# Kernel tuning notes

Measured on AMD Instinct MI355X. Metric: run time of the kernel, lower is better.

## Reference

```python
import jax, jax.numpy as jnp
import numpy as np

B, H0, W0, C = 16, 56, 56, 96
NH, WS, SS = 3, 7, 3
HID, NCL, TAU = 384, 128, 0.5
EPS = 1e-6

def layernorm(x, g, b):
    m = jnp.mean(x, -1, keepdims=True)
    v = jnp.mean((x - m) ** 2, -1, keepdims=True)
    return (x - m) * jax.lax.rsqrt(v + 1e-5) * g + b

def setup_inputs() -> dict:
    key = jax.random.key(0)
    ks = jax.random.split(key, 16)
    s = lambda d: 1.0 / np.sqrt(d)
    return {
        "x": jax.random.normal(ks[0], (B, H0 * W0, C), jnp.float32),
        "norm1_g": jnp.ones((C,)), "norm1_b": jnp.zeros((C,)),
        "qkv_w": jax.random.normal(ks[1], (3 * C, C)) * s(C),
        "qkv_b": jnp.zeros((3 * C,)),
        "proj_w": jax.random.normal(ks[2], (C, C)) * s(C),
        "proj_b": jnp.zeros((C,)),
        "norm2_g": jnp.ones((C,)), "norm2_b": jnp.zeros((C,)),
        "ffn_norm_g": jnp.ones((C,)), "ffn_norm_b": jnp.zeros((C,)),
        "pin_w": jax.random.normal(ks[3], (HID, C)) * s(C),
        "pin_b": jnp.zeros((HID,)),
        "tm_inc": jax.random.normal(ks[4], (NCL, 2 * HID)) * 0.5,
        "tm_out": jax.random.normal(ks[5], (NCL, C)) * s(NCL),
        "gate": jnp.float32(0.5),
        "H": H0, "W": W0,
    }

def window_attention(win, qkv_w, qkv_b, proj_w, proj_b):
    N, T, Cc = win.shape
    hd = Cc // NH
    qkv = win @ qkv_w.T + qkv_b                      # [N, T, 3C]
    qkv = qkv.reshape(N, T, 3, NH, hd).transpose(2, 0, 3, 1, 4)
    q, k, v = qkv[0], qkv[1], qkv[2]                 # [N, nh, T, hd]
    attn = jax.nn.softmax(jnp.einsum('nhqd,nhkd->nhqk', q, k) * (hd ** -0.5), axis=-1)
    out = jnp.einsum('nhqk,nhkd->nhqd', attn, v).transpose(0, 2, 1, 3).reshape(N, T, Cc)
    return out @ proj_w.T + proj_b

def tm_ffn(x, ffn_norm_g, ffn_norm_b, pin_w, pin_b, tm_inc, tm_out, gate):
    # x: [B, T, C]
    Bb, T, Cc = x.shape
    y = jax.nn.sigmoid(layernorm(x, ffn_norm_g, ffn_norm_b) @ pin_w.T + pin_b)  # [B,T,HID]
    flat = y.reshape(Bb * T, HID)
    lits = jnp.clip(jnp.concatenate([flat, 1.0 - flat], axis=-1), EPS, 1.0)     # [N, 2*HID]
    m = jax.nn.sigmoid(tm_inc)
    hard = (m > TAU).astype(m.dtype)
    m_ste = m + jax.lax.stop_gradient(hard - m)      # binary via STE
    # binary mask -> conjunction prod_k l_k^{m_jk} = exp(log(l) @ m^T)
    clauses = jnp.exp(jnp.log(lits) @ m_ste.T)       # [N, NCL]
    logits = (clauses @ tm_out).reshape(Bb, T, Cc)
    g = jax.nn.sigmoid(gate)
    return g * logits + (1.0 - g) * jax.nn.sigmoid(logits)

def reference(x, norm1_g, norm1_b, qkv_w, qkv_b, proj_w, proj_b,
              norm2_g, norm2_b, ffn_norm_g, ffn_norm_b,
              pin_w, pin_b, tm_inc, tm_out, gate, H, W):
    Bb, L, Cc = x.shape
    shortcut = x
    y = layernorm(x, norm1_g, norm1_b).reshape(Bb, H, W, Cc)
    pad_h = (WS - H % WS) % WS
    pad_w = (WS - W % WS) % WS
    if pad_h or pad_w:
        y = jnp.pad(y, ((0, 0), (0, pad_h), (0, pad_w), (0, 0)))
    Hp, Wp = y.shape[1], y.shape[2]
    if SS > 0:
        y = jnp.roll(y, shift=(-SS, -SS), axis=(1, 2))
    # window partition
    y = y.reshape(Bb, Hp // WS, WS, Wp // WS, WS, Cc).transpose(0, 1, 3, 2, 4, 5)
    win = y.reshape(-1, WS * WS, Cc)
    a = window_attention(win, qkv_w, qkv_b, proj_w, proj_b)
    a = a.reshape(Bb, Hp // WS, Wp // WS, WS, WS, Cc)
    if SS > 0:
        a = jnp.roll(a, shift=(SS, SS), axis=(3, 4))
    # window reverse
    a = a.transpose(0, 1, 3, 2, 4, 5).reshape(Bb, Hp, Wp, Cc)
    if pad_h or pad_w:
        a = a[:, :H, :W, :]
    a = a.reshape(Bb, H * W, Cc)
    x1 = shortcut + a
    x2 = x1 + tm_ffn(layernorm(x1, norm2_g, norm2_b),
                     ffn_norm_g, ffn_norm_b, pin_w, pin_b, tm_inc, tm_out, gate)
    return x2
```

## Files before the change

kernel.cpp:

```cpp
#include <hip/hip_runtime.h>

#define NB 16
#define NHH 56
#define NWW 56
#define NC 96
#define NL (NHH*NWW)
#define NTOK (NB*NL)
#define WSZ 7
#define NT 49
#define SSH 3
#define NWIN 1024
#define HDIM 32
#define HID_ 384
#define NCL_ 128
#define NLIT 768
#define EPS_ 1e-6f
#define LOG_EPS -13.815510558f

typedef unsigned short u16;
typedef unsigned int   u32;
typedef __attribute__((ext_vector_type(8))) short short8;
typedef __attribute__((ext_vector_type(4))) float f32x4;

__device__ __forceinline__ float us2f(u16 u) {
  union { u32 u; float f; } x; x.u = ((u32)u) << 16; return x.f;
}
__device__ __forceinline__ u16 f2us(float f) {
  union { float f; u32 u; } x; x.f = f;
  u32 lsb = (x.u >> 16) & 1u;
  return (u16)((x.u + 0x7fffu + lsb) >> 16);
}
__device__ __forceinline__ float sigmoidf_(float x) { return 1.f / (1.f + __expf(-x)); }

__global__ __launch_bounds__(256) void k0_prep(const float* __restrict__ tm_inc,
                                               const float* __restrict__ pin_w,
                                               const float* __restrict__ tm_out,
                                               const float* __restrict__ qkv_w,
                                               const float* __restrict__ proj_w,
                                               u16* __restrict__ maskb,
                                               u16* __restrict__ pinwb,
                                               u16* __restrict__ tmoT,
                                               u16* __restrict__ qkvwb,
                                               u16* __restrict__ projwb) {
  int idx = blockIdx.x * 256 + threadIdx.x;
  if (idx < NCL_ * NLIT) {
    int c = idx / NLIT, q = idx - c * NLIT;
    int j = (q & 1) ? (q >> 1) + HID_ : (q >> 1);
    maskb[idx] = (tm_inc[(size_t)c * NLIT + j] > 0.f) ? (u16)0x3F80 : (u16)0;
  }
  if (idx < HID_ * NC)
    pinwb[idx] = f2us(pin_w[idx]);
  if (idx < NC * NCL_) {
    int c = idx / NCL_, k = idx - c * NCL_;
    tmoT[idx] = f2us(tm_out[(size_t)k * NC + c]);
  }
  if (idx < 3 * NC * NC)
    qkvwb[idx] = f2us(qkv_w[idx]);
  if (idx < NC * NC)
    projwb[idx] = f2us(proj_w[idx]);
}

__global__ __launch_bounds__(256, 4) void k2_attn(const float* __restrict__ x,
                                               const float* __restrict__ n1g,
                                               const float* __restrict__ n1b,
                                               const u16* __restrict__ qkvwb,
                                               const float* __restrict__ qkv_b,
                                               const u16* __restrict__ projwb,
                                               const float* __restrict__ proj_b,
                                               float* __restrict__ x1) {
  __shared__ __align__(16) u16 syb[64 * 104];
  __shared__ __align__(16) u16 sk [64 * 104];
  __shared__ __align__(16) u16 svT[96 * 72];
  const int tid  = threadIdx.x;
  const int wave = tid >> 6;
  const int lane = tid & 63;
  const int l16  = lane & 15;
  const int quad = lane >> 4;
  const int win  = blockIdx.x;
  const int t0   = wave * 16;
  const int bb = win >> 6, wl = win & 63;
  const int hbase = (wl >> 3) * WSZ, wbase = (wl & 7) * WSZ;

  {
    const int t = tid >> 2, s = tid & 3;
    if (t < NT) {
      int hp = hbase + t / WSZ, wp = wbase + t % WSZ;
      int h = hp + SSH; if (h >= NHH) h -= NHH;
      int w = wp + SSH; if (w >= NWW) w -= NWW;
      const float* xp = x + ((size_t)bb * NL + (size_t)h * NWW + w) * NC;
      float4 v[6];
      float sum = 0.f;
      #pragma unroll
      for (int k = 0; k < 6; ++k) {
        v[k] = *reinterpret_cast<const float4*>(xp + s * 4 + k * 16);
        sum += v[k].x + v[k].y + v[k].z + v[k].w;
      }
      sum += __shfl_xor(sum, 1); sum += __shfl_xor(sum, 2);
      float mean = sum * (1.f / 96.f);
      float ssq = 0.f;
      #pragma unroll
      for (int k = 0; k < 6; ++k) {
        float d0 = v[k].x - mean, d1 = v[k].y - mean;
        float d2 = v[k].z - mean, d3 = v[k].w - mean;
        ssq += d0 * d0 + d1 * d1 + d2 * d2 + d3 * d3;
      }
      ssq += __shfl_xor(ssq, 1); ssq += __shfl_xor(ssq, 2);
      float rstd = rsqrtf(ssq * (1.f / 96.f) + 1e-5f);
      #pragma unroll
      for (int k = 0; k < 6; ++k) {
        int c = s * 4 + k * 16;
        const float4 g4 = *reinterpret_cast<const float4*>(n1g + c);
        const float4 b4 = *reinterpret_cast<const float4*>(n1b + c);
        syb[t * 104 + c + 0] = f2us((v[k].x - mean) * rstd * g4.x + b4.x);
        syb[t * 104 + c + 1] = f2us((v[k].y - mean) * rstd * g4.y + b4.y);
        syb[t * 104 + c + 2] = f2us((v[k].z - mean) * rstd * g4.z + b4.z);
        syb[t * 104 + c + 3] = f2us((v[k].w - mean) * rstd * g4.w + b4.w);
      }
    } else {
      #pragma unroll
      for (int k = 0; k < 6; ++k) {
        int c = s * 4 + k * 16;
        syb[t * 104 + c + 0] = 0; syb[t * 104 + c + 1] = 0;
        syb[t * 104 + c + 2] = 0; syb[t * 104 + c + 3] = 0;
      }
    }
  }

  {
    short8 afr[3];
    #pragma unroll
    for (int ks = 0; ks < 3; ++ks)
      afr[ks] = *reinterpret_cast<const short8*>(&syb[(t0 + l16) * 104 + quad * 8 + ks * 32]);
    short8 rb[4][3];
    #pragma unroll
    for (int p = 0; p < 4; ++p)
      #pragma unroll
      for (int ks = 0; ks < 3; ++ks)
        rb[p][ks] = *reinterpret_cast<const short8*>(
            qkvwb + (size_t)(p * 16 + l16) * NC + quad * 8 + ks * 32);
    #pragma unroll
    for (int nt = 0; nt < 18; ++nt) {
      const int n0 = nt * 16;
      const float bias = qkv_b[n0 + l16];
      short8 b0 = rb[nt & 3][0], b1 = rb[nt & 3][1], b2 = rb[nt & 3][2];
      if (nt + 4 < 18) {
        #pragma unroll
        for (int ks = 0; ks < 3; ++ks)
          rb[nt & 3][ks] = *reinterpret_cast<const short8*>(
              qkvwb + (size_t)((nt + 4) * 16 + l16) * NC + quad * 8 + ks * 32);
      }
      f32x4 acc = {0.f, 0.f, 0.f, 0.f};
      acc = __builtin_amdgcn_mfma_f32_16x16x32_bf16(afr[0], b0, acc, 0, 0, 0);
      acc = __builtin_amdgcn_mfma_f32_16x16x32_bf16(afr[1], b1, acc, 0, 0, 0);
      acc = __builtin_amdgcn_mfma_f32_16x16x32_bf16(afr[2], b2, acc, 0, 0, 0);
      const int part = nt / 6;
      const int oc = n0 - part * 96 + l16;
      if (part < 2) {
        u16* dst = (part == 0) ? syb : sk;
        #pragma unroll
        for (int r = 0; r < 4; ++r)
          dst[(t0 + quad * 4 + r) * 104 + oc] = f2us(acc[r] + bias);
      } else {
        #pragma unroll
        for (int r = 0; r < 4; ++r)
          svT[oc * 72 + (t0 + quad * 4 + r)] = f2us(acc[r] + bias);
      }
    }
  }
  __syncthreads();

  u16* spw = sk + wave * 16 * 72;
  const float sscale = 0.17677669529663687f;
  short8 qf[3];
  f32x4 s[3][4];
  #pragma unroll
  for (int h = 0; h < 3; ++h)
    qf[h] = *reinterpret_cast<const short8*>(&syb[(t0 + l16) * 104 + h * HDIM + quad * 8]);
  #pragma unroll
  for (int h = 0; h < 3; ++h) {
    const int d0 = h * HDIM;
    #pragma unroll
    for (int nt = 0; nt < 4; ++nt) {
      short8 kf = *reinterpret_cast<const short8*>(&sk[(nt * 16 + l16) * 104 + d0 + quad * 8]);
      f32x4 a = {0.f, 0.f, 0.f, 0.f};
      s[h][nt] = __builtin_amdgcn_mfma_f32_16x16x32_bf16(qf[h], kf, a, 0, 0, 0);
    }
  }
  __syncthreads();
  #pragma unroll
  for (int h = 0; h < 3; ++h) {
    const int d0 = h * HDIM;
    #pragma unroll
    for (int nt = 0; nt < 4; ++nt)
      #pragma unroll
      for (int r = 0; r < 4; ++r) s[h][nt][r] *= sscale;
    if (l16 >= 1) {
      #pragma unroll
      for (int r = 0; r < 4; ++r) s[h][3][r] = -1e30f;
    }
    #pragma unroll
    for (int r = 0; r < 4; ++r) {
      float m = fmaxf(fmaxf(s[h][0][r], s[h][1][r]), fmaxf(s[h][2][r], s[h][3][r]));
      #pragma unroll
      for (int off = 8; off > 0; off >>= 1) m = fmaxf(m, __shfl_xor(m, off, 16));
      float e0 = __expf(s[h][0][r] - m), e1 = __expf(s[h][1][r] - m);
      float e2 = __expf(s[h][2][r] - m), e3 = __expf(s[h][3][r] - m);
      float sum = e0 + e1 + e2 + e3;
      #pragma unroll
      for (int off = 8; off > 0; off >>= 1) sum += __shfl_xor(sum, off, 16);
      float inv = 1.f / sum;
      const int row = quad * 4 + r;
      spw[row * 72 +      l16] = f2us(e0 * inv);
      spw[row * 72 + 16 + l16] = f2us(e1 * inv);
      spw[row * 72 + 32 + l16] = f2us(e2 * inv);
      spw[row * 72 + 48 + l16] = f2us(e3 * inv);
    }
    short8 pa[2];
    pa[0] = *reinterpret_cast<const short8*>(&spw[l16 * 72 + quad * 8]);
    pa[1] = *reinterpret_cast<const short8*>(&spw[l16 * 72 + 32 + quad * 8]);
    #pragma unroll
    for (int nt = 0; nt < 2; ++nt) {
      const int c0 = d0 + nt * 16;
      f32x4 acc = {0.f, 0.f, 0.f, 0.f};
      #pragma unroll
      for (int ks = 0; ks < 2; ++ks) {
        short8 vb = *reinterpret_cast<const short8*>(&svT[(c0 + l16) * 72 + ks * 32 + quad * 8]);
        acc = __builtin_amdgcn_mfma_f32_16x16x32_bf16(pa[ks], vb, acc, 0, 0, 0);
      }
      #pragma unroll
      for (int r = 0; r < 4; ++r)
        syb[(t0 + quad * 4 + r) * 104 + c0 + l16] = f2us(acc[r]);
    }
  }

  {
    short8 aa[3];
    #pragma unroll
    for (int ks = 0; ks < 3; ++ks)
      aa[ks] = *reinterpret_cast<const short8*>(&syb[(t0 + l16) * 104 + quad * 8 + ks * 32]);

    size_t tokr[4]; bool tval[4];
    #pragma unroll
    for (int r = 0; r < 4; ++r) {
      const int t = t0 + quad * 4 + r;
      tval[r] = (t < NT);
      int rr = t / WSZ + SSH; if (rr >= WSZ) rr -= WSZ;
      int qq = t % WSZ + SSH; if (qq >= WSZ) qq -= WSZ;
      tokr[r] = (size_t)bb * NL + (size_t)(hbase + rr) * NWW + (wbase + qq);
    }
    float xv[6][4];
    #pragma unroll
    for (int nt = 0; nt < 6; ++nt)
      #pragma unroll
      for (int r = 0; r < 4; ++r)
        xv[nt][r] = tval[r] ? x[tokr[r] * NC + nt * 16 + l16] : 0.f;

    short8 pbr[2][3];
    #pragma unroll
    for (int ks = 0; ks < 3; ++ks)
      pbr[0][ks] = *reinterpret_cast<const short8*>(
          projwb + (size_t)l16 * NC + quad * 8 + ks * 32);
    #pragma unroll
    for (int nt = 0; nt < 6; ++nt) {
      const int n0 = nt * 16;
      const float pb = proj_b[n0 + l16];
      short8 b0 = pbr[nt & 1][0], b1 = pbr[nt & 1][1], b2 = pbr[nt & 1][2];
      if (nt + 1 < 6) {
        #pragma unroll
        for (int ks = 0; ks < 3; ++ks)
          pbr[(nt + 1) & 1][ks] = *reinterpret_cast<const short8*>(
              projwb + (size_t)((nt + 1) * 16 + l16) * NC + quad * 8 + ks * 32);
      }
      f32x4 acc = {0.f, 0.f, 0.f, 0.f};
      acc = __builtin_amdgcn_mfma_f32_16x16x32_bf16(aa[0], b0, acc, 0, 0, 0);
      acc = __builtin_amdgcn_mfma_f32_16x16x32_bf16(aa[1], b1, acc, 0, 0, 0);
      acc = __builtin_amdgcn_mfma_f32_16x16x32_bf16(aa[2], b2, acc, 0, 0, 0);
      #pragma unroll
      for (int r = 0; r < 4; ++r) {
        if (tval[r])
          x1[tokr[r] * NC + n0 + l16] = xv[nt][r] + acc[r] + pb;
      }
    }
  }
}

__device__ __forceinline__ short8 lit_pack(f32x4 p, f32x4 pbv) {
  union { short8 s; u32 w[4]; } u;
  #pragma unroll
  for (int r = 0; r < 4; ++r) {
    const float a  = p[r] + pbv[r];
    const float sp = fmaxf(a, 0.f) + __logf(1.f + __expf(-fabsf(a)));
    const u16 lo = f2us(fmaxf(a - sp, LOG_EPS));
    const u16 hi = f2us(fmaxf(-sp,    LOG_EPS));
    u.w[r] = (u32)lo | ((u32)hi << 16);
  }
  return u.s;
}

__device__ __forceinline__ void k4_step(int ks, bool pref,
    const u16* __restrict__ pinwb, const float* __restrict__ pin_b,
    const u16* __restrict__ maskb, int l16, int quad,
    short8 (&pa)[3], f32x4& pbv, short8 (&mb)[8],
    const short8 (&zb)[2][3], f32x4 (&cacc)[2][8]) {
  const short8 a0 = pa[0], a1 = pa[1], a2 = pa[2];
  const f32x4 pb = pbv;
  f32x4 p0 = {0.f, 0.f, 0.f, 0.f}, p1 = {0.f, 0.f, 0.f, 0.f};
  p0 = __builtin_amdgcn_mfma_f32_16x16x32_bf16(a0, zb[0][0], p0, 0, 0, 0);
  p1 = __builtin_amdgcn_mfma_f32_16x16x32_bf16(a0, zb[1][0], p1, 0, 0, 0);
  p0 = __builtin_amdgcn_mfma_f32_16x16x32_bf16(a1, zb[0][1], p0, 0, 0, 0);
  p1 = __builtin_amdgcn_mfma_f32_16x16x32_bf16(a1, zb[1][1], p1, 0, 0, 0);
  p0 = __builtin_amdgcn_mfma_f32_16x16x32_bf16(a2, zb[0][2], p0, 0, 0, 0);
  p1 = __builtin_amdgcn_mfma_f32_16x16x32_bf16(a2, zb[1][2], p1, 0, 0, 0);
  if (pref) {
    const u16* pp = pinwb + (size_t)((ks + 2) * 16 + l16) * NC + quad * 8;
    pa[0] = *reinterpret_cast<const short8*>(pp);
    pa[1] = *reinterpret_cast<const short8*>(pp + 32);
    pa[2] = *reinterpret_cast<const short8*>(pp + 64);
    pbv   = *reinterpret_cast<const f32x4*>(pin_b + (ks + 2) * 16 + quad * 4);
  }
  const short8 lf0 = lit_pack(p0, pb);
  const short8 lf1 = lit_pack(p1, pb);
  #pragma unroll
  for (int ct = 0; ct < 8; ++ct) {
    cacc[0][ct] = __builtin_amdgcn_mfma_f32_16x16x32_bf16(lf0, mb[ct], cacc[0][ct], 0, 0, 0);
    cacc[1][ct] = __builtin_amdgcn_mfma_f32_16x16x32_bf16(lf1, mb[ct], cacc[1][ct], 0, 0, 0);
  }
  if (pref) {
    #pragma unroll
    for (int ct = 0; ct < 8; ++ct)
      mb[ct] = *reinterpret_cast<const short8*>(
          maskb + (size_t)(ct * 16 + l16) * NLIT + (ks + 2) * 32 + quad * 8);
  }
}

__device__ __forceinline__ float sum4_(float4 v) { return (v.x + v.y) + (v.z + v.w); }

__global__ __launch_bounds__(256, 2) void k4_ffn(const float* __restrict__ x1,
                                              const float* __restrict__ g2,
                                              const float* __restrict__ b2,
                                              const float* __restrict__ gf,
                                              const float* __restrict__ bf,
                                              const u16* __restrict__ pinwb,
                                              const float* __restrict__ pin_b,
                                              const u16* __restrict__ maskb,
                                              const u16* __restrict__ tmoT,
                                              const float* __restrict__ gate,
                                              float* __restrict__ out) {
  __shared__ __align__(16) u16 claT_s[4 * 32 * 136];
  const int tid  = threadIdx.x;
  const int wave = tid >> 6;
  const int lane = tid & 63;
  const int l16  = lane & 15;
  const int quad = lane >> 4;
  u16* claT = claT_s + wave * 32 * 136;
  const size_t tok0 = (size_t)blockIdx.x * 128 + wave * 32;

  float4 g2v[3][2], b2v[3][2], gfv[3][2], bfv[3][2];
  #pragma unroll
  for (int k = 0; k < 3; ++k) {
    const int c = k * 32 + quad * 8;
    g2v[k][0] = *reinterpret_cast<const float4*>(g2 + c);
    g2v[k][1] = *reinterpret_cast<const float4*>(g2 + c + 4);
    b2v[k][0] = *reinterpret_cast<const float4*>(b2 + c);
    b2v[k][1] = *reinterpret_cast<const float4*>(b2 + c + 4);
    gfv[k][0] = *reinterpret_cast<const float4*>(gf + c);
    gfv[k][1] = *reinterpret_cast<const float4*>(gf + c + 4);
    bfv[k][0] = *reinterpret_cast<const float4*>(bf + c);
    bfv[k][1] = *reinterpret_cast<const float4*>(bf + c + 4);
  }
  short8 zb[2][3];
  #pragma unroll
  for (int g = 0; g < 2; ++g) {
    const float* xp = x1 + (tok0 + g * 16 + l16) * NC + quad * 8;
    float4 va[3], vb[3];
    float sum = 0.f;
    #pragma unroll
    for (int k = 0; k < 3; ++k) {
      va[k] = *reinterpret_cast<const float4*>(xp + k * 32);
      vb[k] = *reinterpret_cast<const float4*>(xp + k * 32 + 4);
      sum += sum4_(va[k]) + sum4_(vb[k]);
    }
    sum += __shfl_xor(sum, 16); sum += __shfl_xor(sum, 32);
    const float mean = sum * (1.f / 96.f);
    float ssq = 0.f;
    #pragma unroll
    for (int k = 0; k < 3; ++k) {
      float d;
      d = va[k].x - mean; ssq += d * d;  d = va[k].y - mean; ssq += d * d;
      d = va[k].z - mean; ssq += d * d;  d = va[k].w - mean; ssq += d * d;
      d = vb[k].x - mean; ssq += d * d;  d = vb[k].y - mean; ssq += d * d;
      d = vb[k].z - mean; ssq += d * d;  d = vb[k].w - mean; ssq += d * d;
    }
    ssq += __shfl_xor(ssq, 16); ssq += __shfl_xor(ssq, 32);
    const float rstd = rsqrtf(ssq * (1.f / 96.f) + 1e-5f);
    float sum2 = 0.f;
    #pragma unroll
    for (int k = 0; k < 3; ++k) {
      va[k].x = (va[k].x - mean) * rstd * g2v[k][0].x + b2v[k][0].x; sum2 += va[k].x;
      va[k].y = (va[k].y - mean) * rstd * g2v[k][0].y + b2v[k][0].y; sum2 += va[k].y;
      va[k].z = (va[k].z - mean) * rstd * g2v[k][0].z + b2v[k][0].z; sum2 += va[k].z;
      va[k].w = (va[k].w - mean) * rstd * g2v[k][0].w + b2v[k][0].w; sum2 += va[k].w;
      vb[k].x = (vb[k].x - mean) * rstd * g2v[k][1].x + b2v[k][1].x; sum2 += vb[k].x;
      vb[k].y = (vb[k].y - mean) * rstd * g2v[k][1].y + b2v[k][1].y; sum2 += vb[k].y;
      vb[k].z = (vb[k].z - mean) * rstd * g2v[k][1].z + b2v[k][1].z; sum2 += vb[k].z;
      vb[k].w = (vb[k].w - mean) * rstd * g2v[k][1].w + b2v[k][1].w; sum2 += vb[k].w;
    }
    sum2 += __shfl_xor(sum2, 16); sum2 += __shfl_xor(sum2, 32);
    const float mean2 = sum2 * (1.f / 96.f);
    float ssq2 = 0.f;
    #pragma unroll
    for (int k = 0; k < 3; ++k) {
      float d;
      d = va[k].x - mean2; ssq2 += d * d;  d = va[k].y - mean2; ssq2 += d * d;
      d = va[k].z - mean2; ssq2 += d * d;  d = va[k].w - mean2; ssq2 += d * d;
      d = vb[k].x - mean2; ssq2 += d * d;  d = vb[k].y - mean2; ssq2 += d * d;
      d = vb[k].z - mean2; ssq2 += d * d;  d = vb[k].w - mean2; ssq2 += d * d;
    }
    ssq2 += __shfl_xor(ssq2, 16); ssq2 += __shfl_xor(ssq2, 32);
    const float rstd2 = rsqrtf(ssq2 * (1.f / 96.f) + 1e-5f);
    #pragma unroll
    for (int k = 0; k < 3; ++k) {
      const float z0 = (va[k].x - mean2) * rstd2 * gfv[k][0].x + bfv[k][0].x;
      const float z1 = (va[k].y - mean2) * rstd2 * gfv[k][0].y + bfv[k][0].y;
      const float z2 = (va[k].z - mean2) * rstd2 * gfv[k][0].z + bfv[k][0].z;
      const float z3 = (va[k].w - mean2) * rstd2 * gfv[k][0].w + bfv[k][0].w;
      const float z4 = (vb[k].x - mean2) * rstd2 * gfv[k][1].x + bfv[k][1].x;
      const float z5 = (vb[k].y - mean2) * rstd2 * gfv[k][1].y + bfv[k][1].y;
      const float z6 = (vb[k].z - mean2) * rstd2 * gfv[k][1].z + bfv[k][1].z;
      const float z7 = (vb[k].w - mean2) * rstd2 * gfv[k][1].w + bfv[k][1].w;
      union { short8 s; u32 w[4]; } uz;
      uz.w[0] = (u32)f2us(z0) | ((u32)f2us(z1) << 16);
      uz.w[1] = (u32)f2us(z2) | ((u32)f2us(z3) << 16);
      uz.w[2] = (u32)f2us(z4) | ((u32)f2us(z5) << 16);
      uz.w[3] = (u32)f2us(z6) | ((u32)f2us(z7) << 16);
      zb[g][k] = uz.s;
    }
  }

  short8 paA[3], paB[3], mbA[8], mbB[8];
  f32x4 pbvA, pbvB;
  {
    const u16* pp0 = pinwb + (size_t)(l16) * NC + quad * 8;
    const u16* pp1 = pinwb + (size_t)(16 + l16) * NC + quad * 8;
    #pragma unroll
    for (int k = 0; k < 3; ++k) {
      paA[k] = *reinterpret_cast<const short8*>(pp0 + k * 32);
      paB[k] = *reinterpret_cast<const short8*>(pp1 + k * 32);
    }
    pbvA = *reinterpret_cast<const f32x4*>(pin_b + quad * 4);
    pbvB = *reinterpret_cast<const f32x4*>(pin_b + 16 + quad * 4);
    #pragma unroll
    for (int ct = 0; ct < 8; ++ct) {
      const u16* mp = maskb + (size_t)(ct * 16 + l16) * NLIT + quad * 8;
      mbA[ct] = *reinterpret_cast<const short8*>(mp);
      mbB[ct] = *reinterpret_cast<const short8*>(mp + 32);
    }
  }
  f32x4 cacc[2][8];
  {
    const f32x4 z4 = {0.f, 0.f, 0.f, 0.f};
    #pragma unroll
    for (int g = 0; g < 2; ++g)
      #pragma unroll
      for (int ct = 0; ct < 8; ++ct)
        cacc[g][ct] = z4;
  }

  for (int kk = 0; kk < 12; ++kk) {
    k4_step(2 * kk,     kk < 11, pinwb, pin_b, maskb, l16, quad, paA, pbvA, mbA, zb, cacc);
    k4_step(2 * kk + 1, kk < 11, pinwb, pin_b, maskb, l16, quad, paB, pbvB, mbB, zb, cacc);
  }

  float xr[2][6][4];
  #pragma unroll
  for (int g = 0; g < 2; ++g)
    #pragma unroll
    for (int nt = 0; nt < 6; ++nt)
      #pragma unroll
      for (int r = 0; r < 4; ++r)
        xr[g][nt][r] = x1[(tok0 + g * 16 + quad * 4 + r) * NC + nt * 16 + l16];

  #pragma unroll
  for (int g = 0; g < 2; ++g)
    #pragma unroll
    for (int ct = 0; ct < 8; ++ct)
      #pragma unroll
      for (int r = 0; r < 4; ++r)
        claT[(g * 16 + quad * 4 + r) * 136 + ct * 16 + l16] = f2us(__expf(cacc[g][ct][r]));

  short8 caf[2][4];
  #pragma unroll
  for (int g = 0; g < 2; ++g)
    #pragma unroll
    for (int ks = 0; ks < 4; ++ks)
      caf[g][ks] = *reinterpret_cast<const short8*>(
          &claT[(g * 16 + l16) * 136 + ks * 32 + quad * 8]);
  const float gv = sigmoidf_(gate[0]);
  #pragma unroll
  for (int nt = 0; nt < 6; ++nt) {
    short8 btm[4];
    #pragma unroll
    for (int ks = 0; ks < 4; ++ks)
      btm[ks] = *reinterpret_cast<const short8*>(
          tmoT + (size_t)(nt * 16 + l16) * NCL_ + ks * 32 + quad * 8);
    f32x4 o0 = {0.f, 0.f, 0.f, 0.f}, o1 = {0.f, 0.f, 0.f, 0.f};
    #pragma unroll
    for (int ks = 0; ks < 4; ++ks) {
      o0 = __builtin_amdgcn_mfma_f32_16x16x32_bf16(caf[0][ks], btm[ks], o0, 0, 0, 0);
      o1 = __builtin_amdgcn_mfma_f32_16x16x32_bf16(caf[1][ks], btm[ks], o1, 0, 0, 0);
    }
    const int c = nt * 16 + l16;
    #pragma unroll
    for (int r = 0; r < 4; ++r) {
      const float lg0 = o0[r], lg1 = o1[r];
      out[(tok0 + quad * 4 + r) * NC + c]      = xr[0][nt][r] + gv * lg0 + (1.f - gv) * sigmoidf_(lg0);
      out[(tok0 + 16 + quad * 4 + r) * NC + c] = xr[1][nt][r] + gv * lg1 + (1.f - gv) * sigmoidf_(lg1);
    }
  }
}

extern "C" void kernel_launch(void* const* d_in, const int* in_sizes, int n_in,
                              void* d_out, int out_size, void* d_ws, size_t ws_size,
                              hipStream_t stream) {
  (void)in_sizes; (void)n_in; (void)out_size; (void)ws_size;
  const float* x      = (const float*)d_in[0];
  const float* n1g    = (const float*)d_in[1];
  const float* n1b    = (const float*)d_in[2];
  const float* qkv_w  = (const float*)d_in[3];
  const float* qkv_b  = (const float*)d_in[4];
  const float* proj_w = (const float*)d_in[5];
  const float* proj_b = (const float*)d_in[6];
  const float* n2g    = (const float*)d_in[7];
  const float* n2b    = (const float*)d_in[8];
  const float* fng    = (const float*)d_in[9];
  const float* fnb    = (const float*)d_in[10];
  const float* pin_w  = (const float*)d_in[11];
  const float* pin_b  = (const float*)d_in[12];
  const float* tm_inc = (const float*)d_in[13];
  const float* tm_out = (const float*)d_in[14];
  const float* gate   = (const float*)d_in[15];

  float* x1 = (float*)d_ws;
  u16* maskb = (u16*)(x1 + (size_t)NTOK * NC);
  u16* pinwb = maskb + NCL_ * NLIT;
  u16* tmoT  = pinwb + HID_ * NC;
  u16* qkvwb = tmoT + NC * NCL_;
  u16* projwb= qkvwb + 3 * NC * NC;

  hipLaunchKernelGGL(k0_prep, dim3(384), dim3(256), 0, stream,
                     tm_inc, pin_w, tm_out, qkv_w, proj_w, maskb, pinwb, tmoT, qkvwb, projwb);
  hipLaunchKernelGGL(k2_attn, dim3(NWIN), dim3(256), 0, stream,
                     x, n1g, n1b, qkvwb, qkv_b, projwb, proj_b, x1);
  hipLaunchKernelGGL(k4_ffn, dim3(NTOK / 128), dim3(256), 0, stream,
                     x1, n2g, n2b, fng, fnb, pinwb, pin_b, maskb, tmoT, gate, (float*)d_out);
}
```

Baseline: 196.5 us.

## Shrink FFN kernel to one 16-token wave per block, dropping register prefetch

The FFN kernel moves from 256-thread blocks, each wave handling 32 tokens with double-buffered register prefetch of weights and masks, to 64-thread blocks handling 16 tokens each with a plain loop that loads operands each step. LayerNorm parameters are loaded at point of use instead of held in registers. The aim is to cut register pressure and raise occupancy and block count, so more waves hide latency. In exchange, each mask and weight fragment is reused across half as many tokens, which doubles L2 traffic for those operands, and the explicit prefetch pipelining is lost.

```diff
diff --git a/kernel.cpp b/kernel.cpp
--- a/kernel.cpp
+++ b/kernel.cpp
@@ -297,45 +297,9 @@
   return u.s;
 }
 
-__device__ __forceinline__ void k4_step(int ks, bool pref,
-    const u16* __restrict__ pinwb, const float* __restrict__ pin_b,
-    const u16* __restrict__ maskb, int l16, int quad,
-    short8 (&pa)[3], f32x4& pbv, short8 (&mb)[8],
-    const short8 (&zb)[2][3], f32x4 (&cacc)[2][8]) {
-  const short8 a0 = pa[0], a1 = pa[1], a2 = pa[2];
-  const f32x4 pb = pbv;
-  f32x4 p0 = {0.f, 0.f, 0.f, 0.f}, p1 = {0.f, 0.f, 0.f, 0.f};
-  p0 = __builtin_amdgcn_mfma_f32_16x16x32_bf16(a0, zb[0][0], p0, 0, 0, 0);
-  p1 = __builtin_amdgcn_mfma_f32_16x16x32_bf16(a0, zb[1][0], p1, 0, 0, 0);
-  p0 = __builtin_amdgcn_mfma_f32_16x16x32_bf16(a1, zb[0][1], p0, 0, 0, 0);
-  p1 = __builtin_amdgcn_mfma_f32_16x16x32_bf16(a1, zb[1][1], p1, 0, 0, 0);
-  p0 = __builtin_amdgcn_mfma_f32_16x16x32_bf16(a2, zb[0][2], p0, 0, 0, 0);
-  p1 = __builtin_amdgcn_mfma_f32_16x16x32_bf16(a2, zb[1][2], p1, 0, 0, 0);
-  if (pref) {
-    const u16* pp = pinwb + (size_t)((ks + 2) * 16 + l16) * NC + quad * 8;
-    pa[0] = *reinterpret_cast<const short8*>(pp);
-    pa[1] = *reinterpret_cast<const short8*>(pp + 32);
-    pa[2] = *reinterpret_cast<const short8*>(pp + 64);
-    pbv   = *reinterpret_cast<const f32x4*>(pin_b + (ks + 2) * 16 + quad * 4);
-  }
-  const short8 lf0 = lit_pack(p0, pb);
-  const short8 lf1 = lit_pack(p1, pb);
-  #pragma unroll
-  for (int ct = 0; ct < 8; ++ct) {
-    cacc[0][ct] = __builtin_amdgcn_mfma_f32_16x16x32_bf16(lf0, mb[ct], cacc[0][ct], 0, 0, 0);
-    cacc[1][ct] = __builtin_amdgcn_mfma_f32_16x16x32_bf16(lf1, mb[ct], cacc[1][ct], 0, 0, 0);
-  }
-  if (pref) {
-    #pragma unroll
-    for (int ct = 0; ct < 8; ++ct)
-      mb[ct] = *reinterpret_cast<const short8*>(
-          maskb + (size_t)(ct * 16 + l16) * NLIT + (ks + 2) * 32 + quad * 8);
-  }
-}
-
 __device__ __forceinline__ float sum4_(float4 v) { return (v.x + v.y) + (v.z + v.w); }
 
-__global__ __launch_bounds__(256, 2) void k4_ffn(const float* __restrict__ x1,
+__global__ __launch_bounds__(64, 3) void k4_ffn(const float* __restrict__ x1,
                                               const float* __restrict__ g2,
                                               const float* __restrict__ b2,
                                               const float* __restrict__ gf,
@@ -346,32 +310,15 @@
                                               const u16* __restrict__ tmoT,
                                               const float* __restrict__ gate,
                                               float* __restrict__ out) {
-  __shared__ __align__(16) u16 claT_s[4 * 32 * 136];
-  const int tid  = threadIdx.x;
-  const int wave = tid >> 6;
-  const int lane = tid & 63;
+  __shared__ __align__(16) u16 claT[16 * 136];
+  const int lane = threadIdx.x & 63;
   const int l16  = lane & 15;
   const int quad = lane >> 4;
-  u16* claT = claT_s + wave * 32 * 136;
-  const size_t tok0 = (size_t)blockIdx.x * 128 + wave * 32;
-
-  float4 g2v[3][2], b2v[3][2], gfv[3][2], bfv[3][2];
-  #pragma unroll
-  for (int k = 0; k < 3; ++k) {
-    const int c = k * 32 + quad * 8;
-    g2v[k][0] = *reinterpret_cast<const float4*>(g2 + c);
-    g2v[k][1] = *reinterpret_cast<const float4*>(g2 + c + 4);
-    b2v[k][0] = *reinterpret_cast<const float4*>(b2 + c);
-    b2v[k][1] = *reinterpret_cast<const float4*>(b2 + c + 4);
-    gfv[k][0] = *reinterpret_cast<const float4*>(gf + c);
-    gfv[k][1] = *reinterpret_cast<const float4*>(gf + c + 4);
-    bfv[k][0] = *reinterpret_cast<const float4*>(bf + c);
-    bfv[k][1] = *reinterpret_cast<const float4*>(bf + c + 4);
-  }
-  short8 zb[2][3];
-  #pragma unroll
-  for (int g = 0; g < 2; ++g) {
-    const float* xp = x1 + (tok0 + g * 16 + l16) * NC + quad * 8;
+  const size_t tok0 = (size_t)blockIdx.x * 16;
+
+  short8 zb[3];
+  {
+    const float* xp = x1 + (tok0 + l16) * NC + quad * 8;
     float4 va[3], vb[3];
     float sum = 0.f;
     #pragma unroll
@@ -396,14 +343,19 @@
     float sum2 = 0.f;
     #pragma unroll
     for (int k = 0; k < 3; ++k) {
-      va[k].x = (va[k].x - mean) * rstd * g2v[k][0].x + b2v[k][0].x; sum2 += va[k].x;
-      va[k].y = (va[k].y - mean) * rstd * g2v[k][0].y + b2v[k][0].y; sum2 += va[k].y;
-      va[k].z = (va[k].z - mean) * rstd * g2v[k][0].z + b2v[k][0].z; sum2 += va[k].z;
-      va[k].w = (va[k].w - mean) * rstd * g2v[k][0].w + b2v[k][0].w; sum2 += va[k].w;
-      vb[k].x = (vb[k].x - mean) * rstd * g2v[k][1].x + b2v[k][1].x; sum2 += vb[k].x;
-      vb[k].y = (vb[k].y - mean) * rstd * g2v[k][1].y + b2v[k][1].y; sum2 += vb[k].y;
-      vb[k].z = (vb[k].z - mean) * rstd * g2v[k][1].z + b2v[k][1].z; sum2 += vb[k].z;
-      vb[k].w = (vb[k].w - mean) * rstd * g2v[k][1].w + b2v[k][1].w; sum2 += vb[k].w;
+      const int c = k * 32 + quad * 8;
+      const float4 ga = *reinterpret_cast<const float4*>(g2 + c);
+      const float4 gb = *reinterpret_cast<const float4*>(g2 + c + 4);
+      const float4 ba = *reinterpret_cast<const float4*>(b2 + c);
+      const float4 bb = *reinterpret_cast<const float4*>(b2 + c + 4);
+      va[k].x = (va[k].x - mean) * rstd * ga.x + ba.x; sum2 += va[k].x;
+      va[k].y = (va[k].y - mean) * rstd * ga.y + ba.y; sum2 += va[k].y;
+      va[k].z = (va[k].z - mean) * rstd * ga.z + ba.z; sum2 += va[k].z;
+      va[k].w = (va[k].w - mean) * rstd * ga.w + ba.w; sum2 += va[k].w;
+      vb[k].x = (vb[k].x - mean) * rstd * gb.x + bb.x; sum2 += vb[k].x;
+      vb[k].y = (vb[k].y - mean) * rstd * gb.y + bb.y; sum2 += vb[k].y;
+      vb[k].z = (vb[k].z - mean) * rstd * gb.z + bb.z; sum2 += vb[k].z;
+      vb[k].w = (vb[k].w - mean) * rstd * gb.w + bb.w; sum2 += vb[k].w;
     }
     sum2 += __shfl_xor(sum2, 16); sum2 += __shfl_xor(sum2, 32);
     const float mean2 = sum2 * (1.f / 96.f);
@@ -420,101 +372,99 @@
     const float rstd2 = rsqrtf(ssq2 * (1.f / 96.f) + 1e-5f);
     #pragma unroll
     for (int k = 0; k < 3; ++k) {
-      const float z0 = (va[k].x - mean2) * rstd2 * gfv[k][0].x + bfv[k][0].x;
-      const float z1 = (va[k].y - mean2) * rstd2 * gfv[k][0].y + bfv[k][0].y;
-      const float z2 = (va[k].z - mean2) * rstd2 * gfv[k][0].z + bfv[k][0].z;
-      const float z3 = (va[k].w - mean2) * rstd2 * gfv[k][0].w + bfv[k][0].w;
-      const float z4 = (vb[k].x - mean2) * rstd2 * gfv[k][1].x + bfv[k][1].x;
-      const float z5 = (vb[k].y - mean2) * rstd2 * gfv[k][1].y + bfv[k][1].y;
-      const float z6 = (vb[k].z - mean2) * rstd2 * gfv[k][1].z + bfv[k][1].z;
-      const float z7 = (vb[k].w - mean2) * rstd2 * gfv[k][1].w + bfv[k][1].w;
+      const int c = k * 32 + quad * 8;
+      const float4 ga = *reinterpret_cast<const float4*>(gf + c);
+      const float4 gb = *reinterpret_cast<const float4*>(gf + c + 4);
+      const float4 ba = *reinterpret_cast<const float4*>(bf + c);
+      const float4 bb = *reinterpret_cast<const float4*>(bf + c + 4);
+      const float z0 = (va[k].x - mean2) * rstd2 * ga.x + ba.x;
+      const float z1 = (va[k].y - mean2) * rstd2 * ga.y + ba.y;
+      const float z2 = (va[k].z - mean2) * rstd2 * ga.z + ba.z;
+      const float z3 = (va[k].w - mean2) * rstd2 * ga.w + ba.w;
+      const float z4 = (vb[k].x - mean2) * rstd2 * gb.x + bb.x;
+      const float z5 = (vb[k].y - mean2) * rstd2 * gb.y + bb.y;
+      const float z6 = (vb[k].z - mean2) * rstd2 * gb.z + bb.z;
+      const float z7 = (vb[k].w - mean2) * rstd2 * gb.w + bb.w;
       union { short8 s; u32 w[4]; } uz;
       uz.w[0] = (u32)f2us(z0) | ((u32)f2us(z1) << 16);
       uz.w[1] = (u32)f2us(z2) | ((u32)f2us(z3) << 16);
       uz.w[2] = (u32)f2us(z4) | ((u32)f2us(z5) << 16);
       uz.w[3] = (u32)f2us(z6) | ((u32)f2us(z7) << 16);
-      zb[g][k] = uz.s;
-    }
-  }
-
-  short8 paA[3], paB[3], mbA[8], mbB[8];
-  f32x4 pbvA, pbvB;
-  {
-    const u16* pp0 = pinwb + (size_t)(l16) * NC + quad * 8;
-    const u16* pp1 = pinwb + (size_t)(16 + l16) * NC + quad * 8;
-    #pragma unroll
-    for (int k = 0; k < 3; ++k) {
-      paA[k] = *reinterpret_cast<const short8*>(pp0 + k * 32);
-      paB[k] = *reinterpret_cast<const short8*>(pp1 + k * 32);
-    }
-    pbvA = *reinterpret_cast<const f32x4*>(pin_b + quad * 4);
-    pbvB = *reinterpret_cast<const f32x4*>(pin_b + 16 + quad * 4);
-    #pragma unroll
-    for (int ct = 0; ct < 8; ++ct) {
-      const u16* mp = maskb + (size_t)(ct * 16 + l16) * NLIT + quad * 8;
-      mbA[ct] = *reinterpret_cast<const short8*>(mp);
-      mbB[ct] = *reinterpret_cast<const short8*>(mp + 32);
-    }
-  }
-  f32x4 cacc[2][8];
+      zb[k] = uz.s;
+    }
+  }
+
+  f32x4 cacc[8];
   {
     const f32x4 z4 = {0.f, 0.f, 0.f, 0.f};
     #pragma unroll
-    for (int g = 0; g < 2; ++g)
-      #pragma unroll
-      for (int ct = 0; ct < 8; ++ct)
-        cacc[g][ct] = z4;
-  }
-
-  for (int kk = 0; kk < 12; ++kk) {
-    k4_step(2 * kk,     kk < 11, pinwb, pin_b, maskb, l16, quad, paA, pbvA, mbA, zb, cacc);
-    k4_step(2 * kk + 1, kk < 11, pinwb, pin_b, maskb, l16, quad, paB, pbvB, mbB, zb, cacc);
-  }
-
-  float xr[2][6][4];
-  #pragma unroll
-  for (int g = 0; g < 2; ++g)
-    #pragma unroll
-    for (int nt = 0; nt < 6; ++nt)
-      #pragma unroll
-      for (int r = 0; r < 4; ++r)
-        xr[g][nt][r] = x1[(tok0 + g * 16 + quad * 4 + r) * NC + nt * 16 + l16];
-
-  #pragma unroll
-  for (int g = 0; g < 2; ++g)
-    #pragma unroll
-    for (int ct = 0; ct < 8; ++ct)
-      #pragma unroll
-      for (int r = 0; r < 4; ++r)
-        claT[(g * 16 + quad * 4 + r) * 136 + ct * 16 + l16] = f2us(__expf(cacc[g][ct][r]));
-
-  short8 caf[2][4];
-  #pragma unroll
-  for (int g = 0; g < 2; ++g)
-    #pragma unroll
-    for (int ks = 0; ks < 4; ++ks)
-      caf[g][ks] = *reinterpret_cast<const short8*>(
-          &claT[(g * 16 + l16) * 136 + ks * 32 + quad * 8]);
+    for (int ct = 0; ct < 8; ++ct) cacc[ct] = z4;
+  }
+  #pragma unroll 2
+  for (int ks = 0; ks < 24; ++ks) {
+    short8 mb0 = *reinterpret_cast<const short8*>(maskb + (size_t)(0 * 16 + l16) * NLIT + ks * 32 + quad * 8);
+    short8 mb1 = *reinterpret_cast<const short8*>(maskb + (size_t)(1 * 16 + l16) * NLIT + ks * 32 + quad * 8);
+    short8 mb2 = *reinterpret_cast<const short8*>(maskb + (size_t)(2 * 16 + l16) * NLIT + ks * 32 + quad * 8);
+    short8 mb3 = *reinterpret_cast<const short8*>(maskb + (size_t)(3 * 16 + l16) * NLIT + ks * 32 + quad * 8);
+    short8 mb4 = *reinterpret_cast<const short8*>(maskb + (size_t)(4 * 16 + l16) * NLIT + ks * 32 + quad * 8);
+    short8 mb5 = *reinterpret_cast<const short8*>(maskb + (size_t)(5 * 16 + l16) * NLIT + ks * 32 + quad * 8);
+    short8 mb6 = *reinterpret_cast<const short8*>(maskb + (size_t)(6 * 16 + l16) * NLIT + ks * 32 + quad * 8);
+    short8 mb7 = *reinterpret_cast<const short8*>(maskb + (size_t)(7 * 16 + l16) * NLIT + ks * 32 + quad * 8);
+    const u16* pp = pinwb + (size_t)(ks * 16 + l16) * NC + quad * 8;
+    short8 pa0 = *reinterpret_cast<const short8*>(pp);
+    short8 pa1 = *reinterpret_cast<const short8*>(pp + 32);
+    short8 pa2 = *reinterpret_cast<const short8*>(pp + 64);
+    f32x4 pbv = *reinterpret_cast<const f32x4*>(pin_b + ks * 16 + quad * 4);
+    f32x4 p = {0.f, 0.f, 0.f, 0.f};
+    p = __builtin_amdgcn_mfma_f32_16x16x32_bf16(pa0, zb[0], p, 0, 0, 0);
+    p = __builtin_amdgcn_mfma_f32_16x16x32_bf16(pa1, zb[1], p, 0, 0, 0);
+    p = __builtin_amdgcn_mfma_f32_16x16x32_bf16(pa2, zb[2], p, 0, 0, 0);
+    const short8 lf = lit_pack(p, pbv);
+    cacc[0] = __builtin_amdgcn_mfma_f32_16x16x32_bf16(lf, mb0, cacc[0], 0, 0, 0);
+    cacc[1] = __builtin_amdgcn_mfma_f32_16x16x32_bf16(lf, mb1, cacc[1], 0, 0, 0);
+    cacc[2] = __builtin_amdgcn_mfma_f32_16x16x32_bf16(lf, mb2, cacc[2], 0, 0, 0);
+    cacc[3] = __builtin_amdgcn_mfma_f32_16x16x32_bf16(lf, mb3, cacc[3], 0, 0, 0);
+    cacc[4] = __builtin_amdgcn_mfma_f32_16x16x32_bf16(lf, mb4, cacc[4], 0, 0, 0);
+    cacc[5] = __builtin_amdgcn_mfma_f32_16x16x32_bf16(lf, mb5, cacc[5], 0, 0, 0);
+    cacc[6] = __builtin_amdgcn_mfma_f32_16x16x32_bf16(lf, mb6, cacc[6], 0, 0, 0);
+    cacc[7] = __builtin_amdgcn_mfma_f32_16x16x32_bf16(lf, mb7, cacc[7], 0, 0, 0);
+  }
+
+  #pragma unroll
+  for (int ct = 0; ct < 8; ++ct)
+    #pragma unroll
+    for (int r = 0; r < 4; ++r)
+      claT[(quad * 4 + r) * 136 + ct * 16 + l16] = f2us(__expf(cacc[ct][r]));
+
+  float xr[6][4];
+  #pragma unroll
+  for (int nt = 0; nt < 6; ++nt)
+    #pragma unroll
+    for (int r = 0; r < 4; ++r)
+      xr[nt][r] = x1[(tok0 + quad * 4 + r) * NC + nt * 16 + l16];
+
+  short8 caf[4];
+  #pragma unroll
+  for (int ksl = 0; ksl < 4; ++ksl)
+    caf[ksl] = *reinterpret_cast<const short8*>(
+        &claT[l16 * 136 + ksl * 32 + quad * 8]);
   const float gv = sigmoidf_(gate[0]);
   #pragma unroll
   for (int nt = 0; nt < 6; ++nt) {
     short8 btm[4];
     #pragma unroll
-    for (int ks = 0; ks < 4; ++ks)
-      btm[ks] = *reinterpret_cast<const short8*>(
-          tmoT + (size_t)(nt * 16 + l16) * NCL_ + ks * 32 + quad * 8);
-    f32x4 o0 = {0.f, 0.f, 0.f, 0.f}, o1 = {0.f, 0.f, 0.f, 0.f};
-    #pragma unroll
-    for (int ks = 0; ks < 4; ++ks) {
-      o0 = __builtin_amdgcn_mfma_f32_16x16x32_bf16(caf[0][ks], btm[ks], o0, 0, 0, 0);
-      o1 = __builtin_amdgcn_mfma_f32_16x16x32_bf16(caf[1][ks], btm[ks], o1, 0, 0, 0);
-    }
+    for (int ksl = 0; ksl < 4; ++ksl)
+      btm[ksl] = *reinterpret_cast<const short8*>(
+          tmoT + (size_t)(nt * 16 + l16) * NCL_ + ksl * 32 + quad * 8);
+    f32x4 o0 = {0.f, 0.f, 0.f, 0.f};
+    #pragma unroll
+    for (int ksl = 0; ksl < 4; ++ksl)
+      o0 = __builtin_amdgcn_mfma_f32_16x16x32_bf16(caf[ksl], btm[ksl], o0, 0, 0, 0);
     const int c = nt * 16 + l16;
     #pragma unroll
     for (int r = 0; r < 4; ++r) {
-      const float lg0 = o0[r], lg1 = o1[r];
-      out[(tok0 + quad * 4 + r) * NC + c]      = xr[0][nt][r] + gv * lg0 + (1.f - gv) * sigmoidf_(lg0);
-      out[(tok0 + 16 + quad * 4 + r) * NC + c] = xr[1][nt][r] + gv * lg1 + (1.f - gv) * sigmoidf_(lg1);
+      const float lg = o0[r];
+      out[(tok0 + quad * 4 + r) * NC + c] = xr[nt][r] + gv * lg + (1.f - gv) * sigmoidf_(lg);
     }
   }
 }
@@ -551,6 +501,6 @@
                      tm_inc, pin_w, tm_out, qkv_w, proj_w, maskb, pinwb, tmoT, qkvwb, projwb);
   hipLaunchKernelGGL(k2_attn, dim3(NWIN), dim3(256), 0, stream,
                      x, n1g, n1b, qkvwb, qkv_b, projwb, proj_b, x1);
-  hipLaunchKernelGGL(k4_ffn, dim3(NTOK / 128), dim3(256), 0, stream,
+  hipLaunchKernelGGL(k4_ffn, dim3(NTOK / 16), dim3(64), 0, stream,
                      x1, n2g, n2b, fng, fnb, pinwb, pin_b, maskb, tmoT, gate, (float*)d_out);
 }
```

After: 229.7 us. 16.9% more time.
